# Kernel optimization log

Hardware: AMD Instinct MI355X
Metric: run time of the kernel (lower is better)

Reference implementation:

```python
import jax, jax.numpy as jnp
import numpy as np

N = 4096      # nodes
F = 32        # num_features (GATConv in = out per head)
H = 2         # heads
NHID = 64     # per-branch mlp output
C = 10        # num_classes
J = 3         # wavelet filters
E = 65536     # edges (avg degree 16)
G = 13        # num_gat = (3**3 - 1) // 2
NEG_SLOPE = 0.2


def setup_inputs() -> dict:
    key = jax.random.key(0)
    ks = jax.random.split(key, 12)
    sc = np.float32(1.0 / np.sqrt(N))
    g = np.float32(0.1)
    x = jax.random.normal(ks[0], (N, F), jnp.float32)
    edge_index = jax.random.randint(ks[1], (2, E), 0, N)
    U = jax.random.normal(ks[2], (N, N), jnp.float32) * sc
    psi = jax.random.normal(ks[3], (J, N, N), jnp.float32) * sc
    # 13 GATConv(F, F, heads=H) parameter stacks
    gat_W = jax.random.normal(ks[4], (G, F, H * F), jnp.float32) * g
    att_src = jax.random.normal(ks[5], (G, H, F), jnp.float32) * g
    att_dst = jax.random.normal(ks[6], (G, H, F), jnp.float32) * g
    gat_b = jnp.zeros((G, H * F), jnp.float32)
    # 13 branch MLPs: Linear(H*F -> NHID)
    mlp_W = jax.random.normal(ks[7], (G, H * F, NHID), jnp.float32) * g
    mlp_b = jnp.zeros((G, NHID), jnp.float32)
    # final head: Linear(13*NHID -> C)
    out_W = jax.random.normal(ks[8], (G * NHID, C), jnp.float32) * g
    out_b = jnp.zeros((C,), jnp.float32)
    return {"x": x, "edge_index": edge_index, "U": U, "psi": psi,
            "gat_W": gat_W, "att_src": att_src, "att_dst": att_dst,
            "gat_b": gat_b, "mlp_W": mlp_W, "mlp_b": mlp_b,
            "out_W": out_W, "out_b": out_b}


def _gat_branch(coef, W, a_s, a_d, bg, mw, mb, src, dst):
    # GATConv(F, F, heads=H, concat=True) in eval mode, then ELU + Linear.
    h = (coef @ W).reshape(N, H, F)                       # [N,H,F]
    es = jnp.einsum('nhf,hf->nh', h, a_s)                 # src attention logits
    ed = jnp.einsum('nhf,hf->nh', h, a_d)                 # dst attention logits
    e = jax.nn.leaky_relu(es[src] + ed[dst], NEG_SLOPE)   # [E+N,H]
    m = jax.ops.segment_max(e, dst, num_segments=N)       # stable softmax per dst
    w = jnp.exp(e - m[dst])
    z = jax.ops.segment_sum(w, dst, num_segments=N)
    alpha = w / (z[dst] + 1e-16)
    out = jax.ops.segment_sum(alpha[:, :, None] * h[src], dst, num_segments=N)
    out = out.reshape(N, H * F) + bg
    return jax.nn.elu(out) @ mw + mb                      # branch MLP -> [N,NHID]


def reference(x, edge_index, U, psi, gat_W, att_src, att_dst, gat_b,
              mlp_W, mlp_b, out_W, out_b):
    loops = jnp.arange(N)
    src = jnp.concatenate([edge_index[0], loops])         # add_self_loops
    dst = jnp.concatenate([edge_index[1], loops])
    # Scattering tree (layer=3, J=3): 1 + 3 + 9 = 13 coefficient maps.
    af = jnp.abs(x)
    coef0 = U @ af                                        # [N,F]
    y1 = jnp.einsum('jnm,mf->jnf', psi, af)               # level-1 wavelets [J,N,F]
    a1 = jnp.abs(y1)
    coef1 = jnp.einsum('nm,jmf->jnf', U, a1)              # [J,N,F]
    y2 = jnp.einsum('knm,jmf->jknf', psi, a1)             # level-2: psi_k @ |y1_j|
    coef2 = jnp.einsum('nm,jkmf->jknf', U, jnp.abs(y2)).reshape(J * J, N, F)
    coefs = jnp.concatenate([coef0[None], coef1, coef2], axis=0)  # [13,N,F]
    branch = jax.vmap(lambda c, W, a_s, a_d, bg, mw, mb:
                      _gat_branch(c, W, a_s, a_d, bg, mw, mb, src, dst))
    yb = branch(coefs, gat_W, att_src, att_dst, gat_b, mlp_W, mlp_b)  # [13,N,NHID]
    feat = jnp.moveaxis(yb, 0, 1).reshape(N, G * NHID)    # concat branches per node
    logits = jax.nn.elu(feat) @ out_W + out_b             # [N,C]
    return jax.nn.log_softmax(logits, axis=1)
```

## Files before the change

kernel.cpp:

```cpp
#include <hip/hip_runtime.h>
#include <hip/hip_bf16.h>

#define NN 4096
#define FF 32
#define EE 65536
#define GG 13

typedef float floatx4 __attribute__((ext_vector_type(4)));
typedef __bf16 bf16x8 __attribute__((ext_vector_type(8)));
typedef short short8 __attribute__((ext_vector_type(8)));

__device__ inline unsigned short f2bf(float f) {
    unsigned u = __float_as_uint(f);
    u += 0x7FFFu + ((u >> 16) & 1u);
    return (unsigned short)(u >> 16);
}

__device__ inline void gl2lds16(const float* g, float* l) {
    __builtin_amdgcn_global_load_lds(
        (__attribute__((address_space(1))) void*)(void*)(g),
        (__attribute__((address_space(3))) void*)(l), 16, 0, 0);
}


__global__ void k_prep1(const float* __restrict__ x, unsigned short* __restrict__ B) {
    int tid = blockIdx.x * 256 + threadIdx.x;
    int k = tid >> 5, col = tid & 31;
    float v = fabsf(x[tid]);
    B[(((k >> 5) * 2 + (col >> 4)) << 9) + ((col & 15) << 5) + (k & 31)] = f2bf(v);
}

__global__ void k_prep2(const float* __restrict__ P1, unsigned short* __restrict__ B) {
    int tid = blockIdx.x * 256 + threadIdx.x;
    int k = tid / 96, jf = tid % 96;
    int j = jf >> 5, f = jf & 31;
    float v = fabsf(P1[((1 + j) * NN + k) * FF + f]);
    B[(((k >> 5) * 6 + (jf >> 4)) << 9) + ((jf & 15) << 5) + (k & 31)] = f2bf(v);
}

__global__ void k_prep3(const float* __restrict__ P2, unsigned short* __restrict__ B) {
    int tid = blockIdx.x * 256 + threadIdx.x;
    int k = tid / 288, cc = tid % 288;
    int k3 = cc / 96, jf = cc % 96;
    float v = fabsf(P2[((1 + k3) * NN + k) * 96 + jf]);
    B[(((k >> 5) * 18 + (cc >> 4)) << 9) + ((cc & 15) << 5) + (k & 31)] = f2bf(v);
}

__global__ __launch_bounds__(512, 8) void k_pass1(const float* __restrict__ Umat,
                                                  const float* __restrict__ Psi,
                                                  const unsigned short* __restrict__ Bfrag,
                                                  float* __restrict__ Pout,
                                                  unsigned short* __restrict__ Apack) {
    __shared__ float abuf[2][16 * 256];
    __shared__ float cs[2][16 * 32];
    int tile = blockIdx.x, mat = blockIdx.y;
    const float* A = (mat == 0) ? Umat : (Psi + (size_t)(mat - 1) * NN * NN);
    int tid = threadIdx.x;
    int wave = tid >> 6, lane = tid & 63;
    int c15 = lane & 15, q = lane >> 4;

    const float* atile = A + (size_t)tile * 16 * NN;
    const unsigned short* bbase = Bfrag + (c15 << 5) + (q << 3);
    unsigned short* apk = Apack + ((size_t)mat << 24) + (size_t)tile * 65536
                          + (c15 << 5) + (q << 3);

    int r0 = 2 * wave, r1 = 2 * wave + 1;
    const float* g0 = atile + (size_t)r0 * NN + ((lane ^ (r0 & 7)) << 2);
    const float* g1 = atile + (size_t)r1 * NN + ((lane ^ (r1 & 7)) << 2);
    float* l0 = &abuf[0][wave * 512];
    float* l1 = &abuf[1][wave * 512];

    int swz = c15 & 7;
    int u0 = ((wave * 8 + q * 2 + 0) ^ swz) << 2;
    int u1 = ((wave * 8 + q * 2 + 1) ^ swz) << 2;
    int rowbase = c15 << 8;

    floatx4 acc0 = {0.f, 0.f, 0.f, 0.f}, acc1 = {0.f, 0.f, 0.f, 0.f};

    gl2lds16(g0, l0);
    gl2lds16(g1, l0 + 256);
    asm volatile("" ::: "memory");
    short8 pb0 = *(const short8*)(bbase + (size_t)(wave * 2 + 0) * 512);
    short8 pb1 = *(const short8*)(bbase + (size_t)(wave * 2 + 1) * 512);
    asm volatile("s_waitcnt vmcnt(2)" ::: "memory");
    __builtin_amdgcn_s_barrier();
    __builtin_amdgcn_sched_barrier(0);

    for (int c = 0; c < 16; c++) {
        const float* rb = abuf[c & 1];
        if (c < 15) {
            float* wbb = (c & 1) ? l0 : l1;
            gl2lds16(g0 + (size_t)(c + 1) * 256, wbb);
            gl2lds16(g1 + (size_t)(c + 1) * 256, wbb + 256);
        }
        asm volatile("" ::: "memory");
        int ksg = c * 8 + wave;
        floatx4 f0 = *(const floatx4*)(rb + rowbase + u0);
        floatx4 f1 = *(const floatx4*)(rb + rowbase + u1);
        short8 bv0 = pb0, bv1 = pb1;
        if (c < 15) {
            pb0 = *(const short8*)(bbase + (size_t)((ksg + 8) * 2 + 0) * 512);
            pb1 = *(const short8*)(bbase + (size_t)((ksg + 8) * 2 + 1) * 512);
        }
        short8 av;
        av[0]=f2bf(f0[0]); av[1]=f2bf(f0[1]); av[2]=f2bf(f0[2]); av[3]=f2bf(f0[3]);
        av[4]=f2bf(f1[0]); av[5]=f2bf(f1[1]); av[6]=f2bf(f1[2]); av[7]=f2bf(f1[3]);
        *(short8*)(apk + (size_t)ksg * 512) = av;
        bf16x8 ab = __builtin_bit_cast(bf16x8, av);
        acc0 = __builtin_amdgcn_mfma_f32_16x16x32_bf16(ab, __builtin_bit_cast(bf16x8, bv0), acc0, 0, 0, 0);
        acc1 = __builtin_amdgcn_mfma_f32_16x16x32_bf16(ab, __builtin_bit_cast(bf16x8, bv1), acc1, 0, 0, 0);
        if (c < 15) {
            asm volatile("s_waitcnt vmcnt(3)" ::: "memory");
            __builtin_amdgcn_s_barrier();
            __builtin_amdgcn_sched_barrier(0);
        }
    }

    int half = wave & 1;
    floatx4 acc[2] = {acc0, acc1};
    for (int w2 = 0; w2 < 4; w2++) {
        if ((wave >> 1) == w2) {
#pragma unroll
            for (int t = 0; t < 2; t++)
#pragma unroll
                for (int r = 0; r < 4; r++) {
                    int idx = (q * 4 + r) * 32 + t * 16 + c15;
                    if (w2 == 0) cs[half][idx] = acc[t][r];
                    else cs[half][idx] += acc[t][r];
                }
        }
        __syncthreads();
    }
    float* orow = Pout + ((size_t)mat * NN + (size_t)tile * 16) * 32;
    for (int i = tid; i < 16 * 32; i += 512) orow[i] = cs[0][i] + cs[1][i];
}

template <int NT, int NTOT>
__global__ __launch_bounds__(512) void k_passP(const unsigned short* __restrict__ Apack,
                                               const unsigned short* __restrict__ Bfrag,
                                               float* __restrict__ Pout) {
    constexpr int NC = NT * 16;
    constexpr int NCTOT = NTOT * 16;
    int tp = blockIdx.x;
    int mat = blockIdx.y;
    int cg = blockIdx.z;
    int tid = threadIdx.x;
    int wave = tid >> 6, lane = tid & 63;
    int c15 = lane & 15, q = lane >> 4;
    const unsigned short* ap0 = Apack + ((size_t)mat << 24) + (size_t)(2 * tp) * 65536
                                + (size_t)(wave * 16) * 512 + (c15 << 5) + (q << 3);
    const unsigned short* ap1 = ap0 + 65536;
    const unsigned short* bbase = Bfrag + (size_t)(wave * 16) * NTOT * 512
                                  + (size_t)(cg * NT) * 512 + (c15 << 5) + (q << 3);

    floatx4 acc0[NT], acc1[NT];
#pragma unroll
    for (int t = 0; t < NT; t++) {
        acc0[t] = (floatx4){0.f, 0.f, 0.f, 0.f};
        acc1[t] = (floatx4){0.f, 0.f, 0.f, 0.f};
    }

    for (int s = 0; s < 16; s++) {
        short8 a0 = *(const short8*)(ap0 + (size_t)s * 512);
        short8 a1 = *(const short8*)(ap1 + (size_t)s * 512);
        const unsigned short* bp = bbase + (size_t)s * NTOT * 512;
        bf16x8 ab0 = __builtin_bit_cast(bf16x8, a0);
        bf16x8 ab1 = __builtin_bit_cast(bf16x8, a1);
#pragma unroll
        for (int t = 0; t < NT; t++) {
            short8 bv = *(const short8*)(bp + t * 512);
            bf16x8 bb = __builtin_bit_cast(bf16x8, bv);
            acc0[t] = __builtin_amdgcn_mfma_f32_16x16x32_bf16(ab0, bb, acc0[t], 0, 0, 0);
            acc1[t] = __builtin_amdgcn_mfma_f32_16x16x32_bf16(ab1, bb, acc1[t], 0, 0, 0);
        }
    }

    __shared__ float cs[2][16 * NC];
    int half = wave & 1;

#define REDUCE_WRITE(ACC, TILE)                                                   \
    for (int w2 = 0; w2 < 4; w2++) {                                              \
        if ((wave >> 1) == w2) {                                                  \
            _Pragma("unroll")                                                     \
            for (int t = 0; t < NT; t++)                                          \
                _Pragma("unroll")                                                 \
                for (int r = 0; r < 4; r++) {                                     \
                    int idx = (q * 4 + r) * NC + t * 16 + c15;                    \
                    if (w2 == 0) cs[half][idx] = ACC[t][r];                       \
                    else cs[half][idx] += ACC[t][r];                              \
                }                                                                 \
        }                                                                         \
        __syncthreads();                                                          \
    }                                                                             \
    {                                                                             \
        float* orow = Pout + ((size_t)mat * NN + (size_t)(TILE) * 16) * NCTOT     \
                      + cg * NC;                                                  \
        for (int i = tid; i < 16 * NC; i += 512) {                                \
            int r = i / NC, c = i % NC;                                           \
            orow[(size_t)r * NCTOT + c] = cs[0][i] + cs[1][i];                    \
        }                                                                         \
    }

    REDUCE_WRITE(acc0, 2 * tp)
    __syncthreads();
    REDUCE_WRITE(acc1, 2 * tp + 1)
#undef REDUCE_WRITE
}

__global__ void k_hes(const float* __restrict__ P1, const float* __restrict__ P2,
                      const float* __restrict__ P3, const float* __restrict__ gatW,
                      const float* __restrict__ attS, const float* __restrict__ attD,
                      float* __restrict__ h, float* __restrict__ es,
                      float* __restrict__ ed) {
    int w = (blockIdx.x * 256 + threadIdx.x) >> 6;
    int lane = threadIdx.x & 63;
    int g = w >> 12, n = w & 4095;
    const float* crow;
    if (g == 0) crow = P1 + (size_t)n * FF;
    else if (g <= 3) crow = P2 + (size_t)n * 96 + (g - 1) * 32;
    else {
        int j = (g - 4) / 3, k3 = (g - 4) % 3;
        crow = P3 + (size_t)n * 288 + k3 * 96 + j * 32;
    }
    const float* wcol = gatW + g * (32 * 64) + lane;
    float a = 0.f;
#pragma unroll
    for (int f = 0; f < 32; f++) a += crow[f] * wcol[f * 64];
    h[(size_t)w * 64 + lane] = a;
    float vs = a * attS[g * 64 + lane];
    float vd = a * attD[g * 64 + lane];
#pragma unroll
    for (int off = 16; off >= 1; off >>= 1) {
        vs += __shfl_down(vs, off, 32);
        vd += __shfl_down(vd, off, 32);
    }
    if ((lane & 31) == 0) {
        es[w * 2 + (lane >> 5)] = vs;
        ed[w * 2 + (lane >> 5)] = vd;
    }
}

__global__ void k_hist(const int* __restrict__ ei, int* __restrict__ cnt) {
    int e = blockIdx.x * 256 + threadIdx.x;
    int d = (e < EE) ? ei[EE + e] : (e - EE);
    atomicAdd(&cnt[d], 1);
}

__global__ void k_scan(const int* __restrict__ cnt, int* __restrict__ offs,
                       int* __restrict__ cursor) {
    int lane = threadIdx.x;
    int base = lane * 64;
    int s = 0;
    for (int i = 0; i < 64; i++) s += cnt[base + i];
    int x = s;
    for (int d = 1; d < 64; d <<= 1) {
        int y = __shfl_up(x, d);
        if (lane >= d) x += y;
    }
    int run = x - s;
    for (int i = 0; i < 64; i++) {
        offs[base + i] = run;
        cursor[base + i] = run;
        run += cnt[base + i];
    }
}

__global__ void k_scatter(const int* __restrict__ ei, int* __restrict__ cursor,
                          int* __restrict__ csr) {
    int e = blockIdx.x * 256 + threadIdx.x;
    int s, d;
    if (e < EE) { s = ei[e]; d = ei[EE + e]; } else { s = d = e - EE; }
    int pos = atomicAdd(&cursor[d], 1);
    csr[pos] = s;
}

__global__ void k_gat(const float* __restrict__ h, const float* __restrict__ es,
                      const float* __restrict__ ed, const int* __restrict__ offs,
                      const int* __restrict__ cnt, const int* __restrict__ csr,
                      const float* __restrict__ gatb, float* __restrict__ gact) {
    int w = (blockIdx.x * 256 + threadIdx.x) >> 6;
    int lane = threadIdx.x & 63, hh = lane >> 5;
    int g = w >> 12, n = w & 4095;
    float myed = ed[w * 2 + hh];
    float bias = gatb[g * 64 + lane];
    int start = offs[n], deg = cnt[n];
    const float* hg = h + (size_t)g * NN * 64;
    const float* esg = es + (size_t)g * NN * 2;
    int sA = csr[start];
    int sB = (deg > 1) ? csr[start + 1] : 0;
    float hvA = hg[(size_t)sA * 64 + lane];
    float lgA = esg[sA * 2 + hh];
    float m = -INFINITY, z = 0.f, acc = 0.f;
    for (int i = 0; i < deg; i++) {
        int sC = (i + 2 < deg) ? csr[start + i + 2] : 0;
        float hvB = hg[(size_t)sB * 64 + lane];
        float lgB = esg[sB * 2 + hh];
        float lg = lgA + myed;
        lg = (lg > 0.f) ? lg : 0.2f * lg;
        float nm = fmaxf(m, lg);
        float sc = __expf(m - nm);
        float we = __expf(lg - nm);
        z = z * sc + we;
        acc = acc * sc + we * hvA;
        m = nm;
        sA = sB; sB = sC; hvA = hvB; lgA = lgB;
    }
    float o = acc / (z + 1e-16f) + bias;
    o = (o > 0.f) ? o : (__expf(o) - 1.f);
    gact[(size_t)w * 64 + lane] = o;
}

__global__ __launch_bounds__(832) void k_out(const float* __restrict__ gact,
                                             const float* __restrict__ mlpW,
                                             const float* __restrict__ mlpb,
                                             const float* __restrict__ oW,
                                             const float* __restrict__ ob,
                                             float* __restrict__ out) {
    __shared__ float sf[832];
    int n = blockIdx.x;
    int g = threadIdx.x >> 6;
    int k = threadIdx.x & 63;
    const float* grow = gact + ((size_t)g * NN + n) * 64;
    const float* wc = mlpW + (size_t)g * 64 * 64 + k;
    float a = mlpb[g * 64 + k];
#pragma unroll 8
    for (int i = 0; i < 64; i++) a += grow[i] * wc[i * 64];
    a = (a > 0.f) ? a : (__expf(a) - 1.f);
    sf[g * 64 + k] = a;
    __syncthreads();
    if (g == 0) {
        float acc[10];
#pragma unroll
        for (int c = 0; c < 10; c++) acc[c] = 0.f;
#pragma unroll
        for (int i = 0; i < 13; i++) {
            float v = sf[i * 64 + k];
            const float* wp = oW + (i * 64 + k) * 10;
#pragma unroll
            for (int c = 0; c < 10; c++) acc[c] += v * wp[c];
        }
#pragma unroll
        for (int off = 32; off >= 1; off >>= 1)
#pragma unroll
            for (int c = 0; c < 10; c++) acc[c] += __shfl_down(acc[c], off);
        if (k == 0) {
            float m = -INFINITY;
#pragma unroll
            for (int c = 0; c < 10; c++) { acc[c] += ob[c]; m = fmaxf(m, acc[c]); }
            float s = 0.f;
#pragma unroll
            for (int c = 0; c < 10; c++) s += __expf(acc[c] - m);
            float lse = m + __logf(s);
#pragma unroll
            for (int c = 0; c < 10; c++) out[n * 10 + c] = acc[c] - lse;
        }
    }
}

extern "C" void kernel_launch(void* const* d_in, const int* in_sizes, int n_in,
                              void* d_out, int out_size, void* d_ws, size_t ws_size,
                              hipStream_t stream) {
    const float* x    = (const float*)d_in[0];
    const int*   ei   = (const int*)d_in[1];
    const float* U    = (const float*)d_in[2];
    const float* psi  = (const float*)d_in[3];
    const float* gatW = (const float*)d_in[4];
    const float* attS = (const float*)d_in[5];
    const float* attD = (const float*)d_in[6];
    const float* gatb = (const float*)d_in[7];
    const float* mlpW = (const float*)d_in[8];
    const float* mlpb = (const float*)d_in[9];
    const float* oW   = (const float*)d_in[10];
    const float* ob   = (const float*)d_in[11];
    float* out = (float*)d_out;

    char* ws = (char*)d_ws;
    size_t off = 0;
    auto alloc = [&](size_t bytes) { char* p = ws + off; off += (bytes + 255) & ~(size_t)255; return p; };
    unsigned short* Apack = (unsigned short*)alloc((size_t)4 * NN * NN * 2);
    unsigned short* bf1 = (unsigned short*)alloc((size_t)NN * 32 * 2);
    float* P1           = (float*)alloc((size_t)4 * NN * 32 * 4);
    unsigned short* bf2 = (unsigned short*)alloc((size_t)NN * 96 * 2);
    float* P2           = (float*)alloc((size_t)4 * NN * 96 * 4);
    unsigned short* bf3 = (unsigned short*)alloc((size_t)NN * 288 * 2);
    float* P3           = (float*)alloc((size_t)NN * 288 * 4);
    float* h            = (float*)alloc((size_t)GG * NN * 64 * 4);
    float* es           = (float*)alloc((size_t)GG * NN * 2 * 4);
    float* ed           = (float*)alloc((size_t)GG * NN * 2 * 4);
    int* cnt            = (int*)alloc((size_t)NN * 4);
    int* offs           = (int*)alloc((size_t)NN * 4);
    int* cursor         = (int*)alloc((size_t)NN * 4);
    int* csr            = (int*)alloc((size_t)(EE + NN) * 4);
    float* gact         = (float*)alloc((size_t)GG * NN * 64 * 4);
    (void)ws_size; (void)in_sizes; (void)n_in; (void)out_size;

    hipMemsetAsync(cnt, 0, NN * 4, stream);
    k_hist<<<(EE + NN) / 256, 256, 0, stream>>>(ei, cnt);
    k_scan<<<1, 64, 0, stream>>>(cnt, offs, cursor);
    k_scatter<<<(EE + NN) / 256, 256, 0, stream>>>(ei, cursor, csr);

    k_prep1<<<(NN * 32) / 256, 256, 0, stream>>>(x, bf1);
    k_pass1<<<dim3(NN / 16, 4), 512, 0, stream>>>(U, psi, bf1, P1, Apack);
    k_prep2<<<(NN * 96) / 256, 256, 0, stream>>>(P1, bf2);
    k_passP<6, 6><<<dim3(NN / 32, 4, 1), 512, 0, stream>>>(Apack, bf2, P2);
    k_prep3<<<(NN * 288) / 256, 256, 0, stream>>>(P2, bf3);
    k_passP<6, 18><<<dim3(NN / 32, 1, 3), 512, 0, stream>>>(Apack, bf3, P3);

    k_hes<<<(GG * NN * 64) / 256, 256, 0, stream>>>(P1, P2, P3, gatW, attS, attD, h, es, ed);
    k_gat<<<(GG * NN * 64) / 256, 256, 0, stream>>>(h, es, ed, offs, cnt, csr, gatb, gact);
    k_out<<<NN, 832, 0, stream>>>(gact, mlpW, mlpb, oW, ob, out);
}
```

Measured before the change: 627.6 us.

## Replace LDS double-buffered staging with direct batched global loads in pass1

Drops the global_load_lds double buffer with per-chunk barriers in k_pass1. Each lane now reads its A fragments straight from global memory into registers, four k-steps at a time, then converts them to bf16 and issues the MFMAs. This removes the LDS round trip and the block-wide synchronisation on every chunk. In exchange it uses more registers (launch bounds relaxed from 8 to 4 waves per SIMD) and relies on less regular global access patterns, each lane reading 32 bytes per row.

```diff
diff --git a/kernel.cpp b/kernel.cpp
--- a/kernel.cpp
+++ b/kernel.cpp
@@ -14,12 +14,6 @@
     unsigned u = __float_as_uint(f);
     u += 0x7FFFu + ((u >> 16) & 1u);
     return (unsigned short)(u >> 16);
-}
-
-__device__ inline void gl2lds16(const float* g, float* l) {
-    __builtin_amdgcn_global_load_lds(
-        (__attribute__((address_space(1))) void*)(void*)(g),
-        (__attribute__((address_space(3))) void*)(l), 16, 0, 0);
 }
 
 
@@ -46,12 +40,11 @@
     B[(((k >> 5) * 18 + (cc >> 4)) << 9) + ((cc & 15) << 5) + (k & 31)] = f2bf(v);
 }
 
-__global__ __launch_bounds__(512, 8) void k_pass1(const float* __restrict__ Umat,
+__global__ __launch_bounds__(512, 4) void k_pass1(const float* __restrict__ Umat,
                                                   const float* __restrict__ Psi,
                                                   const unsigned short* __restrict__ Bfrag,
                                                   float* __restrict__ Pout,
                                                   unsigned short* __restrict__ Apack) {
-    __shared__ float abuf[2][16 * 256];
     __shared__ float cs[2][16 * 32];
     int tile = blockIdx.x, mat = blockIdx.y;
     const float* A = (mat == 0) ? Umat : (Psi + (size_t)(mat - 1) * NN * NN);
@@ -59,61 +52,40 @@
     int wave = tid >> 6, lane = tid & 63;
     int c15 = lane & 15, q = lane >> 4;
 
-    const float* atile = A + (size_t)tile * 16 * NN;
+    const float* ga = A + ((size_t)tile * 16 + c15) * NN + q * 8;
     const unsigned short* bbase = Bfrag + (c15 << 5) + (q << 3);
     unsigned short* apk = Apack + ((size_t)mat << 24) + (size_t)tile * 65536
                           + (c15 << 5) + (q << 3);
 
-    int r0 = 2 * wave, r1 = 2 * wave + 1;
-    const float* g0 = atile + (size_t)r0 * NN + ((lane ^ (r0 & 7)) << 2);
-    const float* g1 = atile + (size_t)r1 * NN + ((lane ^ (r1 & 7)) << 2);
-    float* l0 = &abuf[0][wave * 512];
-    float* l1 = &abuf[1][wave * 512];
-
-    int swz = c15 & 7;
-    int u0 = ((wave * 8 + q * 2 + 0) ^ swz) << 2;
-    int u1 = ((wave * 8 + q * 2 + 1) ^ swz) << 2;
-    int rowbase = c15 << 8;
-
     floatx4 acc0 = {0.f, 0.f, 0.f, 0.f}, acc1 = {0.f, 0.f, 0.f, 0.f};
 
-    gl2lds16(g0, l0);
-    gl2lds16(g1, l0 + 256);
-    asm volatile("" ::: "memory");
-    short8 pb0 = *(const short8*)(bbase + (size_t)(wave * 2 + 0) * 512);
-    short8 pb1 = *(const short8*)(bbase + (size_t)(wave * 2 + 1) * 512);
-    asm volatile("s_waitcnt vmcnt(2)" ::: "memory");
-    __builtin_amdgcn_s_barrier();
-    __builtin_amdgcn_sched_barrier(0);
-
-    for (int c = 0; c < 16; c++) {
-        const float* rb = abuf[c & 1];
-        if (c < 15) {
-            float* wbb = (c & 1) ? l0 : l1;
-            gl2lds16(g0 + (size_t)(c + 1) * 256, wbb);
-            gl2lds16(g1 + (size_t)(c + 1) * 256, wbb + 256);
-        }
-        asm volatile("" ::: "memory");
-        int ksg = c * 8 + wave;
-        floatx4 f0 = *(const floatx4*)(rb + rowbase + u0);
-        floatx4 f1 = *(const floatx4*)(rb + rowbase + u1);
-        short8 bv0 = pb0, bv1 = pb1;
-        if (c < 15) {
-            pb0 = *(const short8*)(bbase + (size_t)((ksg + 8) * 2 + 0) * 512);
-            pb1 = *(const short8*)(bbase + (size_t)((ksg + 8) * 2 + 1) * 512);
-        }
-        short8 av;
-        av[0]=f2bf(f0[0]); av[1]=f2bf(f0[1]); av[2]=f2bf(f0[2]); av[3]=f2bf(f0[3]);
-        av[4]=f2bf(f1[0]); av[5]=f2bf(f1[1]); av[6]=f2bf(f1[2]); av[7]=f2bf(f1[3]);
-        *(short8*)(apk + (size_t)ksg * 512) = av;
-        bf16x8 ab = __builtin_bit_cast(bf16x8, av);
-        acc0 = __builtin_amdgcn_mfma_f32_16x16x32_bf16(ab, __builtin_bit_cast(bf16x8, bv0), acc0, 0, 0, 0);
-        acc1 = __builtin_amdgcn_mfma_f32_16x16x32_bf16(ab, __builtin_bit_cast(bf16x8, bv1), acc1, 0, 0, 0);
-        if (c < 15) {
-            asm volatile("s_waitcnt vmcnt(3)" ::: "memory");
-            __builtin_amdgcn_s_barrier();
-            __builtin_amdgcn_sched_barrier(0);
-        }
+#pragma unroll
+    for (int grp = 0; grp < 4; grp++) {
+        floatx4 fa0[4], fa1[4];
+        short8 fb0[4], fb1[4];
+#pragma unroll
+        for (int j = 0; j < 4; j++) {
+            int ksg = wave + (grp * 4 + j) * 8;
+            fa0[j] = *(const floatx4*)(ga + ksg * 32);
+            fa1[j] = *(const floatx4*)(ga + ksg * 32 + 4);
+            fb0[j] = *(const short8*)(bbase + (size_t)(ksg * 2 + 0) * 512);
+            fb1[j] = *(const short8*)(bbase + (size_t)(ksg * 2 + 1) * 512);
+        }
+        __builtin_amdgcn_sched_barrier(0);
+#pragma unroll
+        for (int j = 0; j < 4; j++) {
+            int ksg = wave + (grp * 4 + j) * 8;
+            short8 av;
+            av[0]=f2bf(fa0[j][0]); av[1]=f2bf(fa0[j][1]);
+            av[2]=f2bf(fa0[j][2]); av[3]=f2bf(fa0[j][3]);
+            av[4]=f2bf(fa1[j][0]); av[5]=f2bf(fa1[j][1]);
+            av[6]=f2bf(fa1[j][2]); av[7]=f2bf(fa1[j][3]);
+            *(short8*)(apk + (size_t)ksg * 512) = av;
+            bf16x8 ab = __builtin_bit_cast(bf16x8, av);
+            acc0 = __builtin_amdgcn_mfma_f32_16x16x32_bf16(ab, __builtin_bit_cast(bf16x8, fb0[j]), acc0, 0, 0, 0);
+            acc1 = __builtin_amdgcn_mfma_f32_16x16x32_bf16(ab, __builtin_bit_cast(bf16x8, fb1[j]), acc1, 0, 0, 0);
+        }
+        __builtin_amdgcn_sched_barrier(0);
     }
 
     int half = wave & 1;
```

New measurement: 632.8 us. About the same (+0.8%).
